# Performance work log

Measured on AMD Instinct MI355X. Metric: run time of the kernel, lower is better.

The kernel has to match this reference:

```python
import jax, jax.numpy as jnp
import numpy as np

NUM_CLASSES = 10
PIXEL_DIM = 3072  # 3*32*32
N_LAYERS = 3


def setup_inputs() -> dict:
    key = jax.random.key(0)
    k1, k2 = jax.random.split(key)
    x = jax.random.uniform(k1, (512, 3, 32, 32), dtype=jnp.float32)
    # params[c, layer, g] with g = (rz0, ry0, rz1) angles for class-c circuit
    params = jax.random.normal(k2, (NUM_CLASSES, N_LAYERS, 3), dtype=jnp.float32)
    return {"x": x, "params": params}


def _apply_ry(s0, s1, th_half):
    # Ry(t) = [[cos(t/2), -sin(t/2)], [sin(t/2), cos(t/2)]]
    c = jnp.cos(th_half).astype(jnp.complex64)
    s = jnp.sin(th_half).astype(jnp.complex64)
    return c * s0 - s * s1, s * s0 + c * s1


def _apply_rz(s0, s1, th_half):
    # Rz(t) = diag(exp(-i t/2), exp(+i t/2))  (torchquantum convention)
    ph = jnp.exp(-1j * th_half).astype(jnp.complex64)
    return s0 * ph, s1 * jnp.conj(ph)


def reference(x, params):
    B = x.shape[0]
    C = params.shape[0]
    xf = x.reshape(-1)                      # [B*3072] pixel values = Ry encoding angles
    x_half = (0.5 * xf)[None, :]            # broadcast over classes -> [1, N]
    N = xf.shape[0]

    # state |0> per (class, pixel); track the two amplitudes separately
    s0 = jnp.ones((C, N), dtype=jnp.complex64)
    s1 = jnp.zeros((C, N), dtype=jnp.complex64)

    for layer in range(N_LAYERS):
        # data re-uploading: Ry(x)
        s0, s1 = _apply_ry(s0, s1, x_half)
        th = 0.5 * params[:, layer, :]      # [C, 3]
        s0, s1 = _apply_rz(s0, s1, th[:, 0:1])
        s0, s1 = _apply_ry(s0, s1, th[:, 1:2])
        s0, s1 = _apply_rz(s0, s1, th[:, 2:3])

    # MeasureAll(PauliZ): <Z> = |s0|^2 - |s1|^2 ; qout = (<Z>+1)/2 = |s0|^2 (normalized state)
    qout = s0.real ** 2 + s0.imag ** 2      # [C, B*3072]
    return jnp.transpose(qout.reshape(C, B, PIXEL_DIM), (1, 2, 0))  # [B, 3072, C]
```

## Files before the change

### kernel.cpp

```cpp
#include <hip/hip_runtime.h>
#include <math.h>

#define NPIX   (512 * 3072)
#define NCLS   10
#define NLAYER 3
#define PI_4   0.78539816339744830962f

__global__ __launch_bounds__(256) void fused_kernel(const float* __restrict__ x,
                                                    const float* __restrict__ params,
                                                    float* __restrict__ out) {
    __shared__ __align__(16) float y[80];
    __shared__ __align__(16) float coef[72];
    __shared__ __align__(16) float tile[5120];

    const int t = threadIdx.x;
    const int g = blockIdx.x * 256 + t;

    const float2 xv = ((const float2* __restrict__)x)[g];

    if (t < NCLS * 8) {
        const int c = t >> 3;
        const int k = t & 7;
        const float xs = (float)k * PI_4;

        float s0r = 1.f, s0i = 0.f, s1r = 0.f, s1i = 0.f;

        #pragma unroll
        for (int l = 0; l < NLAYER; ++l) {
            {
                float sh, ch;
                sincosf(0.5f * xs, &sh, &ch);
                float n0r = ch * s0r - sh * s1r;
                float n0i = ch * s0i - sh * s1i;
                float n1r = sh * s0r + ch * s1r;
                float n1i = sh * s0i + ch * s1i;
                s0r = n0r; s0i = n0i; s1r = n1r; s1i = n1i;
            }
            {
                float th = 0.5f * params[(c * NLAYER + l) * 3 + 0];
                float st, ct;
                sincosf(th, &st, &ct);
                float n0r = s0r * ct + s0i * st;
                float n0i = s0i * ct - s0r * st;
                float n1r = s1r * ct - s1i * st;
                float n1i = s1i * ct + s1r * st;
                s0r = n0r; s0i = n0i; s1r = n1r; s1i = n1i;
            }
            {
                float th = 0.5f * params[(c * NLAYER + l) * 3 + 1];
                float sh, ch;
                sincosf(th, &sh, &ch);
                float n0r = ch * s0r - sh * s1r;
                float n0i = ch * s0i - sh * s1i;
                float n1r = sh * s0r + ch * s1r;
                float n1i = sh * s0i + ch * s1i;
                s0r = n0r; s0i = n0i; s1r = n1r; s1i = n1i;
            }
            {
                float th = 0.5f * params[(c * NLAYER + l) * 3 + 2];
                float st, ct;
                sincosf(th, &st, &ct);
                float n0r = s0r * ct + s0i * st;
                float n0i = s0i * ct - s0r * st;
                float n1r = s1r * ct - s1i * st;
                float n1i = s1i * ct + s1r * st;
                s0r = n0r; s0i = n0i; s1r = n1r; s1i = n1i;
            }
        }
        y[t] = s0r * s0r + s0i * s0i;
    }
    __syncthreads();

    if (t < NCLS * 7) {
        const int c = t / 7;
        const int j = t % 7;
        float acc = 0.f;
        #pragma unroll
        for (int k = 0; k < 8; ++k) {
            const float ang = (float)k * PI_4;
            float w;
            if (j == 0)       w = 0.125f;
            else if (j <= 3)  w = 0.25f * cosf((float)j * ang);
            else              w = 0.25f * sinf((float)(j - 3) * ang);
            acc += y[c * 8 + k] * w;
        }
        coef[c * 7 + j] = acc;
    }
    __syncthreads();

    float cf[72];
    #pragma unroll
    for (int i = 0; i < 18; ++i)
        ((float4*)cf)[i] = ((const float4*)coef)[i];

    const float px[2] = {xv.x, xv.y};
    float r[20];
    #pragma unroll
    for (int p = 0; p < 2; ++p) {
        float s1, c1;
        __sincosf(px[p], &s1, &c1);
        const float c2 = 2.f * c1 * c1 - 1.f;
        const float s2 = 2.f * s1 * c1;
        const float c3 = c1 * c2 - s1 * s2;
        const float s3 = s1 * c2 + c1 * s2;
        #pragma unroll
        for (int c = 0; c < NCLS; ++c) {
            const float* f = &cf[c * 7];
            r[p * 10 + c] = f[0] + f[1] * c1 + f[2] * c2 + f[3] * c3
                                 + f[4] * s1 + f[5] * s2 + f[6] * s3;
        }
    }

    float4* wb = (float4*)&tile[t * 20];
    #pragma unroll
    for (int i = 0; i < 5; ++i) wb[i] = ((const float4*)r)[i];

    __syncthreads();

    float4* o4 = (float4*)out + (size_t)blockIdx.x * 1280;
    const float4* l4 = (const float4*)tile;
    #pragma unroll
    for (int i = 0; i < 5; ++i) o4[i * 256 + t] = l4[i * 256 + t];
}

extern "C" void kernel_launch(void* const* d_in, const int* in_sizes, int n_in,
                              void* d_out, int out_size, void* d_ws, size_t ws_size,
                              hipStream_t stream) {
    const float* x      = (const float*)d_in[0];
    const float* params = (const float*)d_in[1];
    float* out          = (float*)d_out;
    (void)d_ws; (void)ws_size;

    const int pairs  = NPIX / 2;
    const int blocks = pairs / 256;
    fused_kernel<<<blocks, 256, 0, stream>>>(x, params, out);
}
```

Measured before the change: 87.82 us.

## Use nontemporal loads/stores, constant trig tables, fast sincos, and scalarized coefficients

Input loads and output stores now use nontemporal builtins, so the streaming data is meant to bypass cache retention. Fixed-angle sin/cos values in the per-block coefficient precompute are replaced by constant lookup tables, and the parameter rotations use the fast __sincosf intrinsic. The per-thread coefficient copy from LDS goes through readfirstlane to push the values into scalar registers. The fast intrinsic trades a little precision for lower setup cost. The kernel is bandwidth-bound, so the cache hints are the part most likely to matter.

After: 82.49 us. -6.1%, faster.

```diff
diff --git a/kernel.cpp b/kernel.cpp
--- a/kernel.cpp
+++ b/kernel.cpp
@@ -4,7 +4,22 @@
 #define NPIX   (512 * 3072)
 #define NCLS   10
 #define NLAYER 3
-#define PI_4   0.78539816339744830962f
+
+typedef float v2f __attribute__((ext_vector_type(2)));
+typedef float v4f __attribute__((ext_vector_type(4)));
+
+__device__ __constant__ float SHK[8] = {
+    0.0f, 0.38268343236f, 0.70710678119f, 0.92387953251f,
+    1.0f, 0.92387953251f, 0.70710678119f, 0.38268343236f };
+__device__ __constant__ float CHK[8] = {
+    1.0f, 0.92387953251f, 0.70710678119f, 0.38268343236f,
+    0.0f, -0.38268343236f, -0.70710678119f, -0.92387953251f };
+__device__ __constant__ float CT8[8] = {
+    1.0f, 0.70710678119f, 0.0f, -0.70710678119f,
+    -1.0f, -0.70710678119f, 0.0f, 0.70710678119f };
+__device__ __constant__ float ST8[8] = {
+    0.0f, 0.70710678119f, 1.0f, 0.70710678119f,
+    0.0f, -0.70710678119f, -1.0f, -0.70710678119f };
 
 __global__ __launch_bounds__(256) void fused_kernel(const float* __restrict__ x,
                                                     const float* __restrict__ params,
@@ -16,30 +31,28 @@
     const int t = threadIdx.x;
     const int g = blockIdx.x * 256 + t;
 
-    const float2 xv = ((const float2* __restrict__)x)[g];
+    const v2f xv = __builtin_nontemporal_load(&((const v2f*)x)[g]);
 
     if (t < NCLS * 8) {
         const int c = t >> 3;
         const int k = t & 7;
-        const float xs = (float)k * PI_4;
+        const float shx = SHK[k], chx = CHK[k];
 
         float s0r = 1.f, s0i = 0.f, s1r = 0.f, s1i = 0.f;
 
         #pragma unroll
         for (int l = 0; l < NLAYER; ++l) {
             {
-                float sh, ch;
-                sincosf(0.5f * xs, &sh, &ch);
-                float n0r = ch * s0r - sh * s1r;
-                float n0i = ch * s0i - sh * s1i;
-                float n1r = sh * s0r + ch * s1r;
-                float n1i = sh * s0i + ch * s1i;
+                float n0r = chx * s0r - shx * s1r;
+                float n0i = chx * s0i - shx * s1i;
+                float n1r = shx * s0r + chx * s1r;
+                float n1i = shx * s0i + chx * s1i;
                 s0r = n0r; s0i = n0i; s1r = n1r; s1i = n1i;
             }
             {
                 float th = 0.5f * params[(c * NLAYER + l) * 3 + 0];
                 float st, ct;
-                sincosf(th, &st, &ct);
+                __sincosf(th, &st, &ct);
                 float n0r = s0r * ct + s0i * st;
                 float n0i = s0i * ct - s0r * st;
                 float n1r = s1r * ct - s1i * st;
@@ -49,7 +62,7 @@
             {
                 float th = 0.5f * params[(c * NLAYER + l) * 3 + 1];
                 float sh, ch;
-                sincosf(th, &sh, &ch);
+                __sincosf(th, &sh, &ch);
                 float n0r = ch * s0r - sh * s1r;
                 float n0i = ch * s0i - sh * s1i;
                 float n1r = sh * s0r + ch * s1r;
@@ -59,7 +72,7 @@
             {
                 float th = 0.5f * params[(c * NLAYER + l) * 3 + 2];
                 float st, ct;
-                sincosf(th, &st, &ct);
+                __sincosf(th, &st, &ct);
                 float n0r = s0r * ct + s0i * st;
                 float n0i = s0i * ct - s0r * st;
                 float n1r = s1r * ct - s1i * st;
@@ -77,21 +90,21 @@
         float acc = 0.f;
         #pragma unroll
         for (int k = 0; k < 8; ++k) {
-            const float ang = (float)k * PI_4;
             float w;
             if (j == 0)       w = 0.125f;
-            else if (j <= 3)  w = 0.25f * cosf((float)j * ang);
-            else              w = 0.25f * sinf((float)(j - 3) * ang);
+            else if (j <= 3)  w = 0.25f * CT8[(j * k) & 7];
+            else              w = 0.25f * ST8[((j - 3) * k) & 7];
             acc += y[c * 8 + k] * w;
         }
         coef[c * 7 + j] = acc;
     }
     __syncthreads();
 
-    float cf[72];
+    float cf[NCLS * 7];
     #pragma unroll
-    for (int i = 0; i < 18; ++i)
-        ((float4*)cf)[i] = ((const float4*)coef)[i];
+    for (int i = 0; i < NCLS * 7; ++i)
+        cf[i] = __int_as_float(
+            __builtin_amdgcn_readfirstlane(__float_as_int(coef[i])));
 
     const float px[2] = {xv.x, xv.y};
     float r[20];
@@ -111,16 +124,17 @@
         }
     }
 
-    float4* wb = (float4*)&tile[t * 20];
+    v4f* wb = (v4f*)&tile[t * 20];
     #pragma unroll
-    for (int i = 0; i < 5; ++i) wb[i] = ((const float4*)r)[i];
+    for (int i = 0; i < 5; ++i) wb[i] = ((const v4f*)r)[i];
 
     __syncthreads();
 
-    float4* o4 = (float4*)out + (size_t)blockIdx.x * 1280;
-    const float4* l4 = (const float4*)tile;
+    v4f* o4 = (v4f*)out + (size_t)blockIdx.x * 1280;
+    const v4f* l4 = (const v4f*)tile;
     #pragma unroll
-    for (int i = 0; i < 5; ++i) o4[i * 256 + t] = l4[i * 256 + t];
+    for (int i = 0; i < 5; ++i)
+        __builtin_nontemporal_store(l4[i * 256 + t], &o4[i * 256 + t]);
 }
 
 extern "C" void kernel_launch(void* const* d_in, const int* in_sizes, int n_in,
```
